# Kernel optimization log

Hardware: AMD Instinct MI355X
Metric: run time of the kernel (lower is better)

The kernel has to match this reference:

```python
import jax, jax.numpy as jnp
import numpy as np

B, T, NB = 8, 120, 40
VD, WD = 2053, 300
H, E, NH, HD = 512, 256, 8, 64
SEG, NSEG = 12, 10
IDX = np.round(np.linspace(SEG - 1, T - 1, NSEG)).astype(int)  # segment endpoints


def setup_inputs():
    keys = iter(jax.random.split(jax.random.key(0), 64))
    def w(*shape):
        return jax.random.normal(next(keys), shape, jnp.float32) * 0.02
    z = lambda *s: jnp.zeros(s, jnp.float32)
    return dict(
        videos=jax.random.normal(next(keys), (B, T, NB, VD), jnp.float32),
        sub_glove=jax.random.normal(next(keys), (B, WD), jnp.float32),
        obj_glove=jax.random.normal(next(keys), (B, WD), jnp.float32),
        W_ev=w(VD - 5, E), b_ev=z(E),
        W_el=w(5, E), b_el=z(E),
        W_ew=w(WD, E), b_ew=z(E),
        W_sp1=w(2 * E, E), b_sp1=z(E), w_sp2=w(E),
        W_s2o=w(NB, E), b_s2o=z(E),
        W_o2s=w(NB, E), b_o2s=z(E),
        W_tv=w(H, H), b_tv=z(H),
        Wq=w(H, H), bq=z(H), Wk=w(H, H), bk=z(H), Wv=w(H, H), bv=z(H), Wo=w(H, H), bo=z(H),
        g1=jnp.ones(H, jnp.float32), be1=z(H),
        Wf1=w(H, H), bf1=z(H), Wf2=w(H, H), bf2=z(H),
        g2=jnp.ones(H, jnp.float32), be2=z(H),
        W_tr=w(H, H), b_tr=z(H),
        W_tb1=w(2 * H, H), b_tb1=z(H), w_tb2=w(H),
        W_ih=w(4 * H, H), W_hh=w(4 * H, H), b_ih=z(4 * H), b_hh=z(4 * H),
        W_l1=w(2 * H, H), b_l1=z(H), w_l2=w(H),
    )


def reference(videos, sub_glove, obj_glove, W_ev, b_ev, W_el, b_el, W_ew, b_ew,
              W_sp1, b_sp1, w_sp2, W_s2o, b_s2o, W_o2s, b_o2s, W_tv, b_tv,
              Wq, bq, Wk, bk, Wv, bv, Wo, bo, g1, be1, Wf1, bf1, Wf2, bf2, g2, be2,
              W_tr, b_tr, W_tb1, b_tb1, w_tb2, W_ih, W_hh, b_ih, b_hh, W_l1, b_l1, w_l2):
    relu = jax.nn.relu
    # spatialAtt (vectorized over batch; dropout = identity, eval mode)
    ve = relu(videos[..., :VD - 5] @ W_ev + b_ev) + relu(videos[..., VD - 5:] @ W_el + b_el)  # [B,T,NB,E]
    sub_e = relu(sub_glove @ W_ew + b_ew)  # [B,E]
    obj_e = relu(obj_glove @ W_ew + b_ew)

    def attend(word):  # additive attention over bboxes per frame
        wb = jnp.broadcast_to(word[:, None, None, :], ve.shape)
        s = jnp.tanh(jnp.concatenate([ve, wb], -1) @ W_sp1 + b_sp1) @ w_sp2  # [B,T,NB]
        a = jax.nn.softmax(s, -1)
        return jnp.einsum('btn,btne->bte', a, ve), a

    sub_feat, sub_att = attend(sub_e)
    obj_feat, obj_att = attend(obj_e)
    s2o = relu(sub_att @ W_s2o + b_s2o)  # msg_sub2obj on attention weights [B,T,NB]->[B,T,E]
    o2s = relu(obj_att @ W_o2s + b_o2s)
    ori_x = jnp.concatenate([sub_feat + o2s, obj_feat + s2o], -1)  # [B,T,H]
    rel = jnp.concatenate([sub_e, obj_e], -1)[:, None, :]  # [B,1,H]

    def ln(zz, g, b):
        m = zz.mean(-1, keepdims=True)
        v = jnp.mean((zz - m) ** 2, -1, keepdims=True)
        return (zz - m) * jax.lax.rsqrt(v + 1e-5) * g + b

    # transform_visual + 1-layer post-norm TransformerEncoder (relu FFN, dropout=identity)
    x = relu(ori_x @ W_tv + b_tv)
    q = (x @ Wq + bq).reshape(B, T, NH, HD)
    k = (x @ Wk + bk).reshape(B, T, NH, HD)
    v = (x @ Wv + bv).reshape(B, T, NH, HD)
    att = jax.nn.softmax(jnp.einsum('bqhd,bkhd->bhqk', q, k) / np.float32(np.sqrt(HD)), -1)
    ao = jnp.einsum('bhqk,bkhd->bqhd', att, v).reshape(B, T, H) @ Wo + bo
    x = ln(x + ao, g1, be1)
    x = ln(x + relu(x @ Wf1 + bf1) @ Wf2 + bf2, g2, be2)
    within = x  # [B,T,H]

    seg_in = within[:, IDX, :]  # [B,NSEG,H]
    tr = relu(rel @ W_tr + b_tr)
    ctx = jnp.broadcast_to(tr, seg_in.shape)
    beta2 = jax.nn.softmax(jnp.tanh(jnp.concatenate([seg_in, ctx], -1) @ W_tb1 + b_tb1) @ w_tb2, -1)  # [B,NSEG]

    # torch-convention LSTM (gates i,f,g,o); note attention weights are NOT applied to input (vfeat=input)
    def step(carry, xt):
        h, c = carry
        gates = xt @ W_ih.T + h @ W_hh.T + b_ih + b_hh
        i, f, g_, o = jnp.split(gates, 4, -1)
        c = jax.nn.sigmoid(f) * c + jax.nn.sigmoid(i) * jnp.tanh(g_)
        h = jax.nn.sigmoid(o) * jnp.tanh(c)
        return (h, c), h

    (hT, cT), _ = jax.lax.scan(step, (jnp.zeros((B, H), within.dtype), jnp.zeros((B, H), within.dtype)),
                               seg_in.transpose(1, 0, 2))

    ctx2 = jnp.broadcast_to(hT[:, None, :], within.shape)
    beta1 = jax.nn.softmax(jnp.tanh(jnp.concatenate([within, ctx2], -1) @ W_l1 + b_l1) @ w_l2, -1)  # [B,T]
    temp = beta1 + jnp.repeat(beta2, SEG, axis=1)  # temp[:,i] = beta1[:,i] + beta2[:,i//12]
    output = jnp.einsum('bt,bth->bh', temp, within)  # [B,H]
    return output, hT, cT, sub_att, obj_att, beta1, beta2
```

## Files before the change

### kernel.cpp

```cpp
#include <hip/hip_runtime.h>
#include <cstddef>
#include <cstdint>

#define B_ 8
#define T_ 120
#define NB_ 40
#define VD_ 2053
#define E_ 256
#define H_ 512
#define M_ 38400
#define R_ 960

static constexpr size_t OFF_VE    = 0;
static constexpr size_t OFF_SSUB  = OFF_VE + (size_t)M_ * E_;
static constexpr size_t OFF_SOBJ  = OFF_SSUB + M_;
static constexpr size_t OFF_WBS   = OFF_SOBJ + M_;
static constexpr size_t OFF_WBO   = OFF_WBS + B_ * E_;
static constexpr size_t OFF_TBIAS = OFF_WBO + B_ * E_;
static constexpr size_t OFF_ORIX  = OFF_TBIAS + B_ * H_;
static constexpr size_t OFF_X     = OFF_ORIX + (size_t)R_ * H_;
static constexpr size_t OFF_Q     = OFF_X    + (size_t)R_ * H_;
static constexpr size_t OFF_K     = OFF_Q    + (size_t)R_ * H_;
static constexpr size_t OFF_V     = OFF_K    + (size_t)R_ * H_;
static constexpr size_t OFF_AO    = OFF_V    + (size_t)R_ * H_;
static constexpr size_t OFF_ATTN  = OFF_AO   + (size_t)R_ * H_;
static constexpr size_t OFF_X1    = OFF_ATTN + (size_t)R_ * H_;
static constexpr size_t OFF_F1    = OFF_X1   + (size_t)R_ * H_;
static constexpr size_t OFF_F2    = OFF_F1   + (size_t)R_ * H_;
static constexpr size_t OFF_WIN   = OFF_F2   + (size_t)R_ * H_;
static constexpr size_t OFF_WT    = OFF_WIN  + (size_t)R_ * H_;
static constexpr size_t OFF_Z2    = OFF_WT + (size_t)1024 * 2048;
static constexpr size_t OFF_H0    = OFF_Z2 + 128;
static constexpr size_t OFF_HB    = OFF_H0 + 3 * 4096;
static constexpr size_t OFF_L1    = OFF_HB + B_ * H_;
static constexpr size_t OFF_END0  = OFF_L1 + 960;
static constexpr size_t OFF_WIH   = (OFF_END0 + 3) & ~(size_t)3;
static constexpr size_t OFF_WHH   = OFF_WIH + 524288;
static constexpr size_t OFF_WL1B  = OFF_WHH + 524288;
static constexpr size_t OFF_WINBF = OFF_WL1B + 131072;
static constexpr size_t OFF_VEBF  = OFF_WINBF + 245760;
static constexpr size_t OFF_END   = OFF_VEBF + (size_t)M_ * E_ / 2;

static constexpr size_t O_OUT  = 0;
static constexpr size_t O_HT   = 4096;
static constexpr size_t O_CT   = 8192;
static constexpr size_t O_SATT = 12288;
static constexpr size_t O_OATT = 50688;
static constexpr size_t O_B1   = 89088;
static constexpr size_t O_B2   = 90048;

#define DEVFN __device__ __forceinline__

typedef __attribute__((ext_vector_type(8))) short short8;
typedef __attribute__((ext_vector_type(4))) float f32x4;

DEVFN float sigf(float x) { return 1.0f / (1.0f + __expf(-x)); }

DEVFN float fast_tanh(float x) {
  float e = __expf(2.f * x);
  return 1.f - 2.f / (e + 1.f);
}

DEVFN unsigned short f2bf(float x) {
  unsigned int u = __float_as_uint(x);
  u += 0x7FFFu + ((u >> 16) & 1u);
  return (unsigned short)(u >> 16);
}
DEVFN float bf2f(unsigned short u) { return __uint_as_float((unsigned int)u << 16); }

DEVFN short8 mk8(const float* f) {
  short8 r;
#pragma unroll
  for (int j = 0; j < 8; ++j) r[j] = (short)f2bf(f[j]);
  return r;
}

DEVFN float wredsum(float v) {
#pragma unroll
  for (int m = 32; m; m >>= 1) v += __shfl_xor(v, m);
  return v;
}
DEVFN float wredmax(float v) {
#pragma unroll
  for (int m = 32; m; m >>= 1) v = fmaxf(v, __shfl_xor(v, m));
  return v;
}

__global__ __launch_bounds__(256) void k_zero(float* p, int n) {
  int i = blockIdx.x * 256 + threadIdx.x;
  if (i < n) p[i] = 0.f;
}

__global__ __launch_bounds__(256) void k_small0(
    const float* __restrict__ sub_g, const float* __restrict__ obj_g,
    const float* __restrict__ W_ew, const float* __restrict__ b_ew,
    const float* __restrict__ W_sp1, const float* __restrict__ b_sp1,
    const float* __restrict__ W_tr, const float* __restrict__ b_tr,
    const float* __restrict__ W_tb1, const float* __restrict__ b_tb1,
    float* __restrict__ wbs, float* __restrict__ wbo, float* __restrict__ tbias) {
  int b = blockIdx.x, tid = threadIdx.x;
  __shared__ float sg[300], og[300], se[256], oe[256], trl[512];
  for (int i = tid; i < 300; i += 256) { sg[i] = sub_g[b * 300 + i]; og[i] = obj_g[b * 300 + i]; }
  __syncthreads();
  {
    float a1 = b_ew[tid], a2 = a1;
    for (int w = 0; w < 300; ++w) {
      float we = W_ew[w * 256 + tid];
      a1 += sg[w] * we; a2 += og[w] * we;
    }
    se[tid] = fmaxf(a1, 0.f); oe[tid] = fmaxf(a2, 0.f);
  }
  __syncthreads();
  {
    float a1 = b_sp1[tid], a2 = a1;
    for (int e = 0; e < 256; ++e) {
      float ww = W_sp1[(256 + e) * 256 + tid];
      a1 += se[e] * ww; a2 += oe[e] * ww;
    }
    wbs[b * 256 + tid] = a1; wbo[b * 256 + tid] = a2;
  }
  for (int jj = 0; jj < 2; ++jj) {
    int j = tid + jj * 256;
    float a = b_tr[j];
    for (int i = 0; i < 256; ++i) a += se[i] * W_tr[i * 512 + j];
    for (int i = 0; i < 256; ++i) a += oe[i] * W_tr[(256 + i) * 512 + j];
    trl[j] = fmaxf(a, 0.f);
  }
  __syncthreads();
  for (int jj = 0; jj < 2; ++jj) {
    int j = tid + jj * 256;
    float a = b_tb1[j];
    for (int i = 0; i < 512; ++i) a += trl[i] * W_tb1[(size_t)(512 + i) * 512 + j];
    tbias[b * 512 + j] = a;
  }
}

__global__ __launch_bounds__(256) void k_wprep(
    const float* __restrict__ W_ev, const float* __restrict__ W_tv,
    const float* __restrict__ Wq, const float* __restrict__ Wk,
    const float* __restrict__ Wv, const float* __restrict__ Wo,
    const float* __restrict__ Wf1, const float* __restrict__ Wf2,
    const float* __restrict__ W_sp1, const float* __restrict__ W_l1,
    const float* __restrict__ W_ih, const float* __restrict__ W_hh,
    unsigned short* __restrict__ wevbf, unsigned short* __restrict__ w7bf,
    unsigned short* __restrict__ wsp1bf, unsigned short* __restrict__ wl1bf,
    unsigned short* __restrict__ wihbf, unsigned short* __restrict__ whhbf,
    float* __restrict__ hz) {
  int bid = blockIdx.x, tid = threadIdx.x;
  __shared__ float t[64][65];
  if (bid < 128) {
    int kb = bid >> 2, nb = bid & 3;
#pragma unroll
    for (int i = 0; i < 16; ++i) {
      int idx = tid + 256 * i; int r = idx >> 6, c = idx & 63;
      t[r][c] = W_ev[(size_t)(kb * 64 + r) * 256 + nb * 64 + c];
    }
    __syncthreads();
#pragma unroll
    for (int i = 0; i < 16; ++i) {
      int idx = tid + 256 * i; int n = idx >> 6, kk = idx & 63;
      wevbf[(size_t)(nb * 64 + n) * 2048 + kb * 64 + kk] = f2bf(t[kk][n]);
    }
  } else if (bid < 576) {
    int b2 = bid - 128;
    int wsel = b2 >> 6, sub = b2 & 63;
    int kb = sub >> 3, nb = sub & 7;
    const float* src = wsel == 0 ? W_tv : wsel == 1 ? Wq : wsel == 2 ? Wk
                     : wsel == 3 ? Wv : wsel == 4 ? Wo : wsel == 5 ? Wf1 : Wf2;
    unsigned short* dst = w7bf + (size_t)wsel * 262144;
#pragma unroll
    for (int i = 0; i < 16; ++i) {
      int idx = tid + 256 * i; int r = idx >> 6, c = idx & 63;
      t[r][c] = src[(size_t)(kb * 64 + r) * 512 + nb * 64 + c];
    }
    __syncthreads();
#pragma unroll
    for (int i = 0; i < 16; ++i) {
      int idx = tid + 256 * i; int n = idx >> 6, kk = idx & 63;
      dst[(size_t)(nb * 64 + n) * 512 + kb * 64 + kk] = f2bf(t[kk][n]);
    }
  } else if (bid < 592) {
    int b2 = bid - 576;
    int kb = b2 >> 2, nb = b2 & 3;
#pragma unroll
    for (int i = 0; i < 16; ++i) {
      int idx = tid + 256 * i; int r = idx >> 6, c = idx & 63;
      t[r][c] = W_sp1[(size_t)(kb * 64 + r) * 256 + nb * 64 + c];
    }
    __syncthreads();
#pragma unroll
    for (int i = 0; i < 16; ++i) {
      int idx = tid + 256 * i; int n = idx >> 6, kk = idx & 63;
      wsp1bf[(size_t)(nb * 64 + n) * 256 + kb * 64 + kk] = f2bf(t[kk][n]);
    }
  } else if (bid < 656) {
    int b2 = bid - 592;
    int kb = b2 >> 3, nb = b2 & 7;
#pragma unroll
    for (int i = 0; i < 16; ++i) {
      int idx = tid + 256 * i; int r = idx >> 6, c = idx & 63;
      t[r][c] = W_l1[(size_t)(kb * 64 + r) * 512 + nb * 64 + c];
    }
    __syncthreads();
#pragma unroll
    for (int i = 0; i < 16; ++i) {
      int idx = tid + 256 * i; int n = idx >> 6, kk = idx & 63;
      wl1bf[(size_t)(nb * 64 + n) * 512 + kb * 64 + kk] = f2bf(t[kk][n]);
    }
  } else if (bid < 1680) {
    int i = (bid - 656) * 256 + tid;
    const float* s; unsigned short* d; int off;
    if (i < 131072) { s = W_ih; d = wihbf; off = i * 8; }
    else            { s = W_hh; d = whhbf; off = (i - 131072) * 8; }
    float f[8];
#pragma unroll
    for (int j = 0; j < 8; ++j) f[j] = s[off + j];
    *(short8*)(d + off) = mk8(f);
  } else {
    for (int i = tid; i < 12288; i += 256) hz[i] = 0.f;
  }
}

__global__ __launch_bounds__(256) void k_wconvT(const float* __restrict__ src,
                                                unsigned short* __restrict__ dst,
                                                int K, int N) {
  __shared__ float t[64][65];
  int nblk = N >> 6;
  int kb = blockIdx.x / nblk, nb = blockIdx.x - kb * nblk;
  int tid = threadIdx.x;
#pragma unroll
  for (int i = 0; i < 16; ++i) {
    int idx = tid + 256 * i;
    int r = idx >> 6, c = idx & 63;
    t[r][c] = src[(size_t)(kb * 64 + r) * N + nb * 64 + c];
  }
  __syncthreads();
#pragma unroll
  for (int i = 0; i < 16; ++i) {
    int idx = tid + 256 * i;
    int n = idx >> 6, kk = idx & 63;
    dst[(size_t)(nb * 64 + n) * K + kb * 64 + kk] = f2bf(t[kk][n]);
  }
}

__global__ __launch_bounds__(256) void k_wconv7(
    const float* __restrict__ w0, const float* __restrict__ w1,
    const float* __restrict__ w2, const float* __restrict__ w3,
    const float* __restrict__ w4, const float* __restrict__ w5,
    const float* __restrict__ w6, unsigned short* __restrict__ dstb) {
  __shared__ float t[64][65];
  int wsel = blockIdx.x >> 6, sub = blockIdx.x & 63;
  int kb = sub >> 3, nb = sub & 7;
  const float* src = wsel == 0 ? w0 : wsel == 1 ? w1 : wsel == 2 ? w2
                   : wsel == 3 ? w3 : wsel == 4 ? w4 : wsel == 5 ? w5 : w6;
  unsigned short* dst = dstb + (size_t)wsel * 262144;
  int tid = threadIdx.x;
#pragma unroll
  for (int i = 0; i < 16; ++i) {
    int idx = tid + 256 * i;
    int r = idx >> 6, c = idx & 63;
    t[r][c] = src[(size_t)(kb * 64 + r) * 512 + nb * 64 + c];
  }
  __syncthreads();
#pragma unroll
  for (int i = 0; i < 16; ++i) {
    int idx = tid + 256 * i;
    int n = idx >> 6, kk = idx & 63;
    dst[(size_t)(nb * 64 + n) * 512 + kb * 64 + kk] = f2bf(t[kk][n]);
  }
}

__global__ __launch_bounds__(256) void k_cvt2(const float* __restrict__ a,
                                              const float* __restrict__ b,
                                              unsigned short* __restrict__ da,
                                              unsigned short* __restrict__ db) {
  int i = blockIdx.x * 256 + threadIdx.x;
  const float* s; unsigned short* d; int off;
  if (i < 131072) { s = a; d = da; off = i * 8; }
  else            { s = b; d = db; off = (i - 131072) * 8; }
  float f[8];
#pragma unroll
  for (int j = 0; j < 8; ++j) f[j] = s[off + j];
  *(short8*)(d + off) = mk8(f);
}

__global__ __launch_bounds__(512) void k_gemm_ve_m97(
    const float* __restrict__ videos, const unsigned short* __restrict__ wtbf,
    const float* __restrict__ bev, const float* __restrict__ Wel,
    const float* __restrict__ bel, unsigned short* __restrict__ vebf) {
  __shared__ __align__(16) unsigned short lds[20480];
  int tid = threadIdx.x;
  int rowbase = blockIdx.x * 64;
  int lane = tid & 63, wid = tid >> 6;
  int l16 = lane & 15, lk = lane >> 4;

  int arow = tid >> 3, akc = tid & 7;
  const float* apA = videos + (size_t)(rowbase + arow) * VD_ + akc * 8;
  int dstA = arow * 64 + ((akc ^ (arow & 7)) * 8);
  const unsigned short* spB[4];
  int dstB[4];
#pragma unroll
  for (int i = 0; i < 4; ++i) {
    int g = tid + 512 * i;
    int n = g >> 3, kc = g & 7;
    spB[i] = wtbf + (size_t)n * 2048 + kc * 8;
    dstB[i] = 4096 + n * 64 + ((kc ^ (n & 7)) * 8);
  }
  float fa[8];
  short8 stB[4];
#pragma unroll
  for (int j = 0; j < 8; ++j) fa[j] = apA[j];
#pragma unroll
  for (int i = 0; i < 4; ++i) stB[i] = *(const short8*)(spB[i]);

  f32x4 acc[4][2] = {};
  for (int k0 = 0; k0 < 2048; k0 += 64) {
    short8 ha = mk8(fa);
    __syncthreads();
    *(short8*)(lds + dstA) = ha;
#pragma unroll
    for (int i = 0; i < 4; ++i) *(short8*)(lds + dstB[i]) = stB[i];
    __syncthreads();
    int kn = (k0 + 64 < 2048) ? k0 + 64 : 0;
#pragma unroll
    for (int j = 0; j < 8; ++j) fa[j] = apA[kn + j];
#pragma unroll
    for (int i = 0; i < 4; ++i) stB[i] = *(const short8*)(spB[i] + kn);
#pragma unroll
    for (int kk = 0; kk < 2; ++kk) {
      short8 a8[4], b8[2];
#pragma unroll
      for (int fm = 0; fm < 4; ++fm) {
        int row = fm * 16 + l16;
        a8[fm] = *(const short8*)(lds + row * 64 + (((kk * 4 + lk) ^ (row & 7)) * 8));
      }
#pragma unroll
      for (int fn = 0; fn < 2; ++fn) {
        int n = wid * 32 + fn * 16 + l16;
        b8[fn] = *(const short8*)(lds + 4096 + n * 64 + (((kk * 4 + lk) ^ (n & 7)) * 8));
      }
#pragma unroll
      for (int fm = 0; fm < 4; ++fm)
#pragma unroll
        for (int fn = 0; fn < 2; ++fn)
          acc[fm][fn] = __builtin_amdgcn_mfma_f32_16x16x32_bf16(
              a8[fm], b8[fn], acc[fm][fn], 0, 0, 0);
    }
  }
  float bevv[2], belv[2], w5[5][2];
#pragma unroll
  for (int fn = 0; fn < 2; ++fn) {
    int col = wid * 32 + fn * 16 + l16;
    bevv[fn] = bev[col]; belv[fn] = bel[col];
#pragma unroll
    for (int kk = 0; kk < 5; ++kk) w5[kk][fn] = Wel[kk * 256 + col];
  }
#pragma unroll
  for (int fm = 0; fm < 4; ++fm) {
#pragma unroll
    for (int r = 0; r < 4; ++r) {
      int grow = rowbase + fm * 16 + lk * 4 + r;
      const float* vt = videos + (size_t)grow * VD_ + 2048;
      float t0 = vt[0], t1 = vt[1], t2 = vt[2], t3 = vt[3], t4 = vt[4];
      unsigned short* vob = vebf + (size_t)grow * 256;
#pragma unroll
      for (int fn = 0; fn < 2; ++fn) {
        int col = wid * 32 + fn * 16 + l16;
        float s2 = belv[fn] + t0 * w5[0][fn] + t1 * w5[1][fn] + t2 * w5[2][fn] +
                   t3 * w5[3][fn] + t4 * w5[4][fn];
        float vvv = fmaxf(acc[fm][fn][r] + bevv[fn], 0.f) + fmaxf(s2, 0.f);
        vob[col] = f2bf(vvv);
      }
    }
  }
}

__global__ __launch_bounds__(256) void k_score_bf(
    const unsigned short* __restrict__ vebf, const unsigned short* __restrict__ wsp1,
    const float* __restrict__ w_sp2, const float* __restrict__ wbs,
    const float* __restrict__ wbo, float* __restrict__ s_sub,
    float* __restrict__ s_obj) {
  __shared__ float reds[4][64], redo_[4][64];
  int tid = threadIdx.x;
  int rowbase = blockIdx.x * 64;
  int lane = tid & 63, wid = tid >> 6;
  int l16 = lane & 15, lk = lane >> 4;
  const unsigned short* ap[4];
  const unsigned short* bp[4];
#pragma unroll
  for (int fm = 0; fm < 4; ++fm)
    ap[fm] = vebf + (size_t)(rowbase + fm * 16 + l16) * 256 + lk * 8;
#pragma unroll
  for (int fn = 0; fn < 4; ++fn)
    bp[fn] = wsp1 + (size_t)(wid * 64 + fn * 16 + l16) * 256 + lk * 8;
  f32x4 acc[4][4] = {};
#pragma unroll 2
  for (int k0 = 0; k0 < 256; k0 += 32) {
    short8 a8[4], b8[4];
#pragma unroll
    for (int fm = 0; fm < 4; ++fm) a8[fm] = *(const short8*)(ap[fm] + k0);
#pragma unroll
    for (int fn = 0; fn < 4; ++fn) b8[fn] = *(const short8*)(bp[fn] + k0);
#pragma unroll
    for (int fm = 0; fm < 4; ++fm)
#pragma unroll
      for (int fn = 0; fn < 4; ++fn)
        acc[fm][fn] = __builtin_amdgcn_mfma_f32_16x16x32_bf16(
            a8[fm], b8[fn], acc[fm][fn], 0, 0, 0);
  }
  int b = rowbase / 4800;
  float w2[4], bs[4], bo[4];
#pragma unroll
  for (int fn = 0; fn < 4; ++fn) {
    int col = wid * 64 + fn * 16 + l16;
    w2[fn] = w_sp2[col];
    bs[fn] = wbs[b * 256 + col];
    bo[fn] = wbo[b * 256 + col];
  }
  float ps[4][4], po[4][4];
#pragma unroll
  for (int fm = 0; fm < 4; ++fm)
#pragma unroll
    for (int r = 0; r < 4; ++r) {
      float aps = 0, apo = 0;
#pragma unroll
      for (int fn = 0; fn < 4; ++fn) {
        float t = acc[fm][fn][r];
        aps += fast_tanh(t + bs[fn]) * w2[fn];
        apo += fast_tanh(t + bo[fn]) * w2[fn];
      }
      ps[fm][r] = aps;
      po[fm][r] = apo;
    }
#pragma unroll
  for (int m = 1; m < 16; m <<= 1) {
#pragma unroll
    for (int fm = 0; fm < 4; ++fm)
#pragma unroll
      for (int r = 0; r < 4; ++r) {
        ps[fm][r] += __shfl_xor(ps[fm][r], m);
        po[fm][r] += __shfl_xor(po[fm][r], m);
      }
  }
  if (l16 == 0) {
#pragma unroll
    for (int fm = 0; fm < 4; ++fm)
#pragma unroll
      for (int r = 0; r < 4; ++r) {
        int row = fm * 16 + lk * 4 + r;
        reds[wid][row] = ps[fm][r];
        redo_[wid][row] = po[fm][r];
      }
  }
  __syncthreads();
  if (tid < 64) {
    float s1 = reds[0][tid] + reds[1][tid] + reds[2][tid] + reds[3][tid];
    float s2 = redo_[0][tid] + redo_[1][tid] + redo_[2][tid] + redo_[3][tid];
    s_sub[rowbase + tid] = s1;
    s_obj[rowbase + tid] = s2;
  }
}

__global__ __launch_bounds__(256) void k_attend_bf(
    const float* __restrict__ s_sub, const float* __restrict__ s_obj,
    const unsigned short* __restrict__ vebf, const float* __restrict__ W_s2o,
    const float* __restrict__ b_s2o, const float* __restrict__ W_o2s,
    const float* __restrict__ b_o2s, float* __restrict__ out_satt,
    float* __restrict__ out_oatt, float* __restrict__ orix) {
  int row = blockIdx.x;
  int tid = threadIdx.x;
  __shared__ float alds[2][40];
  int wv = tid >> 6, lane = tid & 63;
  if (wv < 2) {
    const float* sarr = (wv ? s_obj : s_sub) + row * 40;
    float v = (lane < 40) ? sarr[lane] : -1e30f;
    float mx = wredmax(v);
    float e = (lane < 40) ? __expf(v - mx) : 0.f;
    float sm = wredsum(e);
    float p = e / sm;
    if (lane < 40) {
      alds[wv][lane] = p;
      (wv ? out_oatt : out_satt)[row * 40 + lane] = p;
    }
  }
  __syncthreads();
  int e = tid;
  const unsigned short* vrow = vebf + (size_t)row * 40 * 256;
  float sf = 0, of = 0, s2o = b_s2o[e], o2s = b_o2s[e];
  for (int n = 0; n < 40; ++n) {
    float as = alds[0][n], aob = alds[1][n];
    float vv = bf2f(vrow[n * 256 + e]);
    sf += as * vv;
    of += aob * vv;
    s2o += as * W_s2o[n * 256 + e];
    o2s += aob * W_o2s[n * 256 + e];
  }
  s2o = fmaxf(s2o, 0.f);
  o2s = fmaxf(o2s, 0.f);
  orix[(size_t)row * 512 + e] = sf + o2s;
  orix[(size_t)row * 512 + 256 + e] = of + s2o;
}

__global__ __launch_bounds__(256) void k_gemm_ve_mfma(
    const float* __restrict__ videos, const unsigned short* __restrict__ wtbf,
    const float* __restrict__ bev, const float* __restrict__ Wel,
    const float* __restrict__ bel, float* __restrict__ ve) {
  int tid = threadIdx.x;
  int rowbase = blockIdx.x * 64;
  int lane = tid & 63, wid = tid >> 6;
  int l16 = lane & 15, lk = lane >> 4;
  const float* ap[4];
  const unsigned short* bp[4];
#pragma unroll
  for (int fm = 0; fm < 4; ++fm)
    ap[fm] = videos + (size_t)(rowbase + fm * 16 + l16) * VD_ + lk * 8;
#pragma unroll
  for (int fn = 0; fn < 4; ++fn)
    bp[fn] = wtbf + (size_t)(wid * 64 + fn * 16 + l16) * 2048 + lk * 8;
  f32x4 acc[4][4] = {};
  for (int k0 = 0; k0 < 2048; k0 += 64) {
// ... 120 lines not shown
    float p = e / sm;
    if (lane < 40) {
      alds[wv][lane] = p;
      (wv ? out_oatt : out_satt)[row * 40 + lane] = p;
    }
  }
  __syncthreads();
  int e = tid;
  const float* vrow = ve + (size_t)row * 40 * 256;
  float sf = 0, of = 0, s2o = b_s2o[e], o2s = b_o2s[e];
  for (int n = 0; n < 40; ++n) {
    float as = alds[0][n], aob = alds[1][n];
    float vv = vrow[n * 256 + e];
    sf += as * vv;
    of += aob * vv;
    s2o += as * W_s2o[n * 256 + e];
    o2s += aob * W_o2s[n * 256 + e];
  }
  s2o = fmaxf(s2o, 0.f);
  o2s = fmaxf(o2s, 0.f);
  orix[(size_t)row * 512 + e] = sf + o2s;
  orix[(size_t)row * 512 + 256 + e] = of + s2o;
}

__global__ __launch_bounds__(256) void k_gemm_h(
    const float* __restrict__ A, const unsigned short* __restrict__ WT,
    const float* __restrict__ b0, const float* __restrict__ b1,
    const float* __restrict__ b2, float* __restrict__ Cbase, int ntiles,
    int relu) {
  int tid = threadIdx.x;
  int bid = blockIdx.x;
  int mt = bid / ntiles, nt = bid - mt * ntiles;
  int rowbase = mt * 64;
  int lane = tid & 63, wid = tid >> 6;
  int wrow = wid >> 1, wcol = wid & 1;
  int l16 = lane & 15, lk = lane >> 4;
  const float* ap[2];
  const unsigned short* bp[2];
#pragma unroll
  for (int fm = 0; fm < 2; ++fm)
    ap[fm] = A + (size_t)(rowbase + wrow * 32 + fm * 16 + l16) * 512 + lk * 8;
#pragma unroll
  for (int fn = 0; fn < 2; ++fn)
    bp[fn] = WT + (size_t)(nt * 64 + wcol * 32 + fn * 16 + l16) * 512 + lk * 8;
  f32x4 acc[2][2] = {};
  for (int k0 = 0; k0 < 512; k0 += 64) {
#pragma unroll
    for (int kk = 0; kk < 2; ++kk) {
      int ko = k0 + kk * 32;
      short8 a8[2], b8[2];
#pragma unroll
      for (int fm = 0; fm < 2; ++fm) {
        float4 x = *(const float4*)(ap[fm] + ko);
        float4 y = *(const float4*)(ap[fm] + ko + 4);
        float f[8] = {x.x, x.y, x.z, x.w, y.x, y.y, y.z, y.w};
        a8[fm] = mk8(f);
      }
#pragma unroll
      for (int fn = 0; fn < 2; ++fn) b8[fn] = *(const short8*)(bp[fn] + ko);
#pragma unroll
      for (int fm = 0; fm < 2; ++fm)
#pragma unroll
        for (int fn = 0; fn < 2; ++fn)
          acc[fm][fn] = __builtin_amdgcn_mfma_f32_16x16x32_bf16(
              a8[fm], b8[fn], acc[fm][fn], 0, 0, 0);
    }
  }
#pragma unroll
  for (int fn = 0; fn < 2; ++fn) {
    int cg = nt * 64 + wcol * 32 + fn * 16 + l16;
    int third = cg >> 9, c = cg & 511;
    const float* bb = third == 0 ? b0 : (third == 1 ? b1 : b2);
    float bv = bb[c];
    float* outp = Cbase + (size_t)third * ((size_t)R_ * H_);
#pragma unroll
    for (int fm = 0; fm < 2; ++fm) {
#pragma unroll
      for (int r = 0; r < 4; ++r) {
        int grow = rowbase + wrow * 32 + fm * 16 + lk * 4 + r;
        float v = acc[fm][fn][r] + bv;
        if (relu) v = fmaxf(v, 0.f);
        outp[(size_t)grow * 512 + c] = v;
      }
    }
  }
}

__global__ __launch_bounds__(256) void k_xproj(
    const float* __restrict__ win, const unsigned short* __restrict__ wih,
    const float* __restrict__ b_ih, const float* __restrict__ b_hh,
    float* __restrict__ gx) {
  int bid = blockIdx.x;
  int mt = bid >> 5, nt = bid & 31;
  int tid = threadIdx.x;
  int lane = tid & 63, wid = tid >> 6;
  int wrow = wid >> 1, wcol = wid & 1;
  int l16 = lane & 15, lk = lane >> 4;
  const float* ap[2];
  bool av[2];
#pragma unroll
  for (int fm = 0; fm < 2; ++fm) {
    int base = mt * 64 + wrow * 32 + fm * 16;
    av[fm] = base < 80;
    int grow = base + l16;
    int s = grow >> 3, b = grow & 7;
    ap[fm] = av[fm] ? (win + (size_t)(b * 120 + 11 + 12 * s) * 512 + lk * 8)
                    : win;
  }
  const unsigned short* bp[2];
#pragma unroll
  for (int fn = 0; fn < 2; ++fn)
    bp[fn] = wih + (size_t)(nt * 64 + wcol * 32 + fn * 16 + l16) * 512 + lk * 8;
  f32x4 acc[2][2] = {};
  for (int k0 = 0; k0 < 512; k0 += 64) {
#pragma unroll
    for (int kk = 0; kk < 2; ++kk) {
      int ko = k0 + kk * 32;
      short8 a8[2], b8[2];
#pragma unroll
      for (int fm = 0; fm < 2; ++fm) {
        if (av[fm]) {
          float4 x = *(const float4*)(ap[fm] + ko);
          float4 y = *(const float4*)(ap[fm] + ko + 4);
          float f[8] = {x.x, x.y, x.z, x.w, y.x, y.y, y.z, y.w};
          a8[fm] = mk8(f);
        } else {
          a8[fm] = short8{0, 0, 0, 0, 0, 0, 0, 0};
        }
      }
#pragma unroll
      for (int fn = 0; fn < 2; ++fn) b8[fn] = *(const short8*)(bp[fn] + ko);
#pragma unroll
      for (int fm = 0; fm < 2; ++fm)
#pragma unroll
        for (int fn = 0; fn < 2; ++fn)
          acc[fm][fn] = __builtin_amdgcn_mfma_f32_16x16x32_bf16(
              a8[fm], b8[fn], acc[fm][fn], 0, 0, 0);
    }
  }
#pragma unroll
  for (int fn = 0; fn < 2; ++fn) {
    int cg = nt * 64 + wcol * 32 + fn * 16 + l16;
    float bv = b_ih[cg] + b_hh[cg];
#pragma unroll
    for (int fm = 0; fm < 2; ++fm) {
      if (!av[fm]) continue;
#pragma unroll
      for (int r = 0; r < 4; ++r) {
        int grow = mt * 64 + wrow * 32 + fm * 16 + lk * 4 + r;
        if (grow < 80) gx[(size_t)grow * 2048 + cg] = acc[fm][fn][r] + bv;
      }
    }
  }
}

__global__ __launch_bounds__(128) void k_lstm_step(
    const float* __restrict__ hin, const unsigned short* __restrict__ whh,
    const float* __restrict__ gx, int s, float* __restrict__ hout,
    float* __restrict__ c_st) {
  int jb = blockIdx.x;
  int tid = threadIdx.x;
  int lane = tid & 63, kw = tid >> 6;
  int l16 = lane & 15, lk = lane >> 4;
  const float* ap = hin + (size_t)l16 * 512 + kw * 256 + lk * 8;
  const unsigned short* bp[4];
#pragma unroll
  for (int fn = 0; fn < 4; ++fn)
    bp[fn] = whh + (size_t)(fn * 512 + jb * 16 + l16) * 512 + kw * 256 + lk * 8;
  f32x4 acc[4] = {};
  for (int k0 = 0; k0 < 256; k0 += 64) {
#pragma unroll
    for (int kk = 0; kk < 2; ++kk) {
      int ko = k0 + kk * 32;
      float4 x = *(const float4*)(ap + ko);
      float4 y = *(const float4*)(ap + ko + 4);
      float f[8] = {x.x, x.y, x.z, x.w, y.x, y.y, y.z, y.w};
      short8 a8 = mk8(f);
#pragma unroll
      for (int fn = 0; fn < 4; ++fn) {
        short8 b8 = *(const short8*)(bp[fn] + ko);
        acc[fn] = __builtin_amdgcn_mfma_f32_16x16x32_bf16(a8, b8, acc[fn], 0, 0, 0);
      }
    }
  }
  __shared__ float part[4][64][4];
  if (kw == 1) {
#pragma unroll
    for (int fn = 0; fn < 4; ++fn)
#pragma unroll
      for (int r = 0; r < 4; ++r) part[fn][lane][r] = acc[fn][r];
  }
  __syncthreads();
  if (kw == 0 && lk < 2) {
    int j = jb * 16 + l16;
#pragma unroll
    for (int r = 0; r < 4; ++r) {
      int b = lk * 4 + r;
      const float* g = gx + (size_t)(s * 8 + b) * 2048;
      float gi = acc[0][r] + part[0][lane][r] + g[j];
      float gf = acc[1][r] + part[1][lane][r] + g[512 + j];
      float gg = acc[2][r] + part[2][lane][r] + g[1024 + j];
      float go = acc[3][r] + part[3][lane][r] + g[1536 + j];
      float c = sigf(gf) * c_st[b * 512 + j] + sigf(gi) * fast_tanh(gg);
      c_st[b * 512 + j] = c;
      hout[b * 512 + j] = sigf(go) * fast_tanh(c);
    }
  }
}

__global__ __launch_bounds__(256) void k_mha(const float* __restrict__ qb,
                                             const float* __restrict__ kb,
                                             const float* __restrict__ vb,
                                             float* __restrict__ ao) {
  int bh = blockIdx.x & 63, qc = blockIdx.x >> 6;
  int b = bh >> 3, h = bh & 7;
  __shared__ float ks[120 * 65];
  __shared__ float vs[120 * 65];
  __shared__ float ps[4][128];
  int tid = threadIdx.x;
  for (int i = 0; i < 30; ++i) {
    int idx = tid + 256 * i;
    int t = idx >> 6, d = idx & 63;
    size_t g = (size_t)(b * 120 + t) * 512 + h * 64 + d;
    ks[t * 65 + d] = kb[g];
    vs[t * 65 + d] = vb[g];
  }
  __syncthreads();
  int wv = tid >> 6, lane = tid & 63;
  for (int i = qc * 30 + wv; i < qc * 30 + 30; i += 4) {
    const float* qrow = qb + (size_t)(b * 120 + i) * 512 + h * 64;
    float s1 = 0, s2 = 0;
    for (int d = 0; d < 64; ++d) {
      float qd = qrow[d];
      s1 += qd * ks[lane * 65 + d];
      if (lane < 56) s2 += qd * ks[(lane + 64) * 65 + d];
    }
    s1 *= 0.125f;
    s2 *= 0.125f;
    if (lane >= 56) s2 = -1e30f;
    float mx = wredmax(fmaxf(s1, s2));
    float e1 = __expf(s1 - mx);
    float e2 = (lane < 56) ? __expf(s2 - mx) : 0.f;
    float sm = wredsum(e1 + e2);
    ps[wv][lane] = e1;
    ps[wv][64 + lane] = e2;
    float o = 0;
    for (int j = 0; j < 120; ++j) o += ps[wv][j] * vs[j * 65 + lane];
    ao[(size_t)(b * 120 + i) * 512 + h * 64 + lane] = o / sm;
  }
}

__global__ __launch_bounds__(256) void k_ln(const float* __restrict__ a,
                                            const float* __restrict__ bsrc,
                                            const float* __restrict__ g,
                                            const float* __restrict__ be,
                                            float* __restrict__ out,
                                            unsigned short* __restrict__ bfout) {
  int row = blockIdx.x * 4 + (threadIdx.x >> 6);
  int lane = threadIdx.x & 63;
  const float* pa = a + (size_t)row * 512;
  const float* pb = bsrc + (size_t)row * 512;
  float z[8];
  float s = 0;
#pragma unroll
  for (int ii = 0; ii < 8; ++ii) {
    int e = lane + 64 * ii;
    z[ii] = pa[e] + pb[e];
    s += z[ii];
  }
  float mean = wredsum(s) * (1.f / 512.f);
  float v = 0;
#pragma unroll
  for (int ii = 0; ii < 8; ++ii) {
    float d = z[ii] - mean;
    v += d * d;
  }
  float rstd = rsqrtf(wredsum(v) * (1.f / 512.f) + 1e-5f);
#pragma unroll
  for (int ii = 0; ii < 8; ++ii) {
    int e = lane + 64 * ii;
    float val = (z[ii] - mean) * rstd * g[e] + be[e];
    out[(size_t)row * 512 + e] = val;
    if (bfout) bfout[(size_t)row * 512 + e] = f2bf(val);
  }
}

__global__ __launch_bounds__(256) void k_hbias(const float* __restrict__ hT,
                                               const float* __restrict__ W_l1,
                                               const float* __restrict__ b_l1,
                                               float* __restrict__ hb) {
  int b = blockIdx.x >> 1, half = blockIdx.x & 1;
  int tid = threadIdx.x;
  __shared__ float hl[512];
  for (int i = tid; i < 512; i += 256) hl[i] = hT[b * 512 + i];
  __syncthreads();
  int j = half * 256 + tid;
  float a = b_l1[j];
  for (int i = 0; i < 512; ++i) a += hl[i] * W_l1[(size_t)(512 + i) * 512 + j];
  hb[b * 512 + j] = a;
}

__global__ __launch_bounds__(256) void k_beta2(
    const float* __restrict__ within, const float* __restrict__ W_tb1,
    const float* __restrict__ w_tb2, const float* __restrict__ tbias,
    float* __restrict__ z2) {
  int bid = blockIdx.x;
// ... 98 lines not shown
  __syncthreads();
  float v[4] = {0, 0, 0, 0};
  for (int jj = 0; jj < 2; ++jj) {
    int j = tid + jj * 256;
    float hbv = hb[b * 512 + j];
    float a0 = hbv, a1 = hbv, a2 = hbv, a3 = hbv;
    for (int i = 0; i < 512; ++i) {
      float ww = W_l1[(size_t)i * 512 + j];
      a0 += xr[0][i] * ww;
      a1 += xr[1][i] * ww;
      a2 += xr[2][i] * ww;
      a3 += xr[3][i] * ww;
    }
    float wl = w_l2[j];
    v[0] += fast_tanh(a0) * wl;
    v[1] += fast_tanh(a1) * wl;
    v[2] += fast_tanh(a2) * wl;
    v[3] += fast_tanh(a3) * wl;
  }
#pragma unroll
  for (int r = 0; r < 4; ++r) red[r][tid] = v[r];
  __syncthreads();
  for (int s = 128; s; s >>= 1) {
    if (tid < s)
      for (int r = 0; r < 4; ++r) red[r][tid] += red[r][tid + s];
    __syncthreads();
  }
  if (tid < 4) l1[r0 + tid] = red[tid][0];
}

__global__ __launch_bounds__(256) void k_final(
    const float* __restrict__ l1, const float* __restrict__ z2,
    const float* __restrict__ within, const float* __restrict__ hT,
    const float* __restrict__ cT, float* __restrict__ dout) {
  int b = blockIdx.x;
  int tid = threadIdx.x;
  __shared__ float temp[120];
  __shared__ float b2[10];
  int wv = tid >> 6, lane = tid & 63;
  if (wv == 1) {
    float v = (lane < 10) ? z2[b * 10 + lane] : -1e30f;
    float mx = wredmax(v);
    float e = (lane < 10) ? __expf(v - mx) : 0.f;
    float sm = wredsum(e);
    if (lane < 10) {
      float p = e / sm;
      b2[lane] = p;
      dout[O_B2 + b * 10 + lane] = p;
    }
  }
  if (wv == 0) {
    float v1 = l1[b * 120 + lane];
    float v2 = (lane + 64 < 120) ? l1[b * 120 + 64 + lane] : -1e30f;
    float mx = wredmax(fmaxf(v1, v2));
    float e1 = __expf(v1 - mx);
    float e2 = (lane + 64 < 120) ? __expf(v2 - mx) : 0.f;
    float sm = wredsum(e1 + e2);
    float p1 = e1 / sm;
    dout[O_B1 + b * 120 + lane] = p1;
    temp[lane] = p1;
    if (lane + 64 < 120) {
      float p2 = e2 / sm;
      dout[O_B1 + b * 120 + 64 + lane] = p2;
      temp[64 + lane] = p2;
    }
  }
  __syncthreads();
  for (int t = tid; t < 120; t += 256) temp[t] += b2[t / 12];
  __syncthreads();
  for (int hh = tid; hh < 512; hh += 256) {
    float o = 0;
    for (int t = 0; t < 120; ++t) o += temp[t] * within[(size_t)(b * 120 + t) * 512 + hh];
    dout[O_OUT + b * 512 + hh] = o;
    dout[O_HT + b * 512 + hh] = hT[b * 512 + hh];
    dout[O_CT + b * 512 + hh] = cT[b * 512 + hh];
  }
}

extern "C" void kernel_launch(void* const* d_in, const int* in_sizes, int n_in,
                              void* d_out, int out_size, void* d_ws, size_t ws_size,
                              hipStream_t stream) {
  const float* videos = (const float*)d_in[0];
  const float* sub_g  = (const float*)d_in[1];
  const float* obj_g  = (const float*)d_in[2];
  const float* W_ev   = (const float*)d_in[3];
  const float* b_ev   = (const float*)d_in[4];
  const float* W_el   = (const float*)d_in[5];
  const float* b_el   = (const float*)d_in[6];
  const float* W_ew   = (const float*)d_in[7];
  const float* b_ew   = (const float*)d_in[8];
  const float* W_sp1  = (const float*)d_in[9];
  const float* b_sp1  = (const float*)d_in[10];
  const float* w_sp2  = (const float*)d_in[11];
  const float* W_s2o  = (const float*)d_in[12];
  const float* b_s2o  = (const float*)d_in[13];
  const float* W_o2s  = (const float*)d_in[14];
  const float* b_o2s  = (const float*)d_in[15];
  const float* W_tv   = (const float*)d_in[16];
  const float* b_tv   = (const float*)d_in[17];
  const float* Wq     = (const float*)d_in[18];
  const float* bq     = (const float*)d_in[19];
  const float* Wk     = (const float*)d_in[20];
  const float* bk     = (const float*)d_in[21];
  const float* Wv     = (const float*)d_in[22];
  const float* bv     = (const float*)d_in[23];
  const float* Wo     = (const float*)d_in[24];
  const float* bo     = (const float*)d_in[25];
  const float* g1     = (const float*)d_in[26];
  const float* be1    = (const float*)d_in[27];
  const float* Wf1    = (const float*)d_in[28];
  const float* bf1    = (const float*)d_in[29];
  const float* Wf2    = (const float*)d_in[30];
  const float* bf2    = (const float*)d_in[31];
  const float* g2     = (const float*)d_in[32];
  const float* be2    = (const float*)d_in[33];
  const float* W_tr   = (const float*)d_in[34];
  const float* b_tr   = (const float*)d_in[35];
  const float* W_tb1  = (const float*)d_in[36];
  const float* b_tb1  = (const float*)d_in[37];
  const float* w_tb2  = (const float*)d_in[38];
  const float* W_ih   = (const float*)d_in[39];
  const float* W_hh   = (const float*)d_in[40];
  const float* b_ih   = (const float*)d_in[41];
  const float* b_hh   = (const float*)d_in[42];
  const float* W_l1   = (const float*)d_in[43];
  const float* b_l1   = (const float*)d_in[44];
  const float* w_l2   = (const float*)d_in[45];

  float* out = (float*)d_out;
  float* w = (float*)d_ws;

  float* ve_p   = w + OFF_VE;
  float* ssub_p = w + OFF_SSUB;
  float* sobj_p = w + OFF_SOBJ;
  float* wbs_p  = w + OFF_WBS;
  float* wbo_p  = w + OFF_WBO;
  float* tb_p   = w + OFF_TBIAS;
  float* orix_p = w + OFF_ORIX;
  float* x_p    = w + OFF_X;
  float* q_p    = w + OFF_Q;
  float* k_p    = w + OFF_K;
  float* v_p    = w + OFF_V;
  float* ao_p   = w + OFF_AO;
  float* attn_p = w + OFF_ATTN;
  float* x1_p   = w + OFF_X1;
  float* f1_p   = w + OFF_F1;
  float* f2_p   = w + OFF_F2;
  float* win_p  = w + OFF_WIN;
  float* z2_p   = w + OFF_Z2;
  float* h_p    = w + OFF_H0;
  float* c_p    = h_p + 2 * 4096;
  float* hb_p   = w + OFF_HB;
  float* l1_p   = w + OFF_L1;

  unsigned short* wtbase = (unsigned short*)(w + OFF_WT);
  unsigned short* wevbf = wtbase;
  unsigned short* w7bf  = wtbase + 524288;
  unsigned short* wtvbf = w7bf;
  unsigned short* wqbf  = w7bf + 1 * 262144;
  unsigned short* wobf  = w7bf + 4 * 262144;
  unsigned short* wf1bf = w7bf + 5 * 262144;
  unsigned short* wf2bf = w7bf + 6 * 262144;
  unsigned short* wsp1bf = w7bf + 7 * 262144;
  unsigned short* wihbf  = (unsigned short*)(w + OFF_WIH);
  unsigned short* whhbf  = (unsigned short*)(w + OFF_WHH);
  unsigned short* wl1bf  = (unsigned short*)(w + OFF_WL1B);
  unsigned short* winbf_p = (unsigned short*)(w + OFF_WINBF);
  unsigned short* vebf_p = (unsigned short*)(w + OFF_VEBF);
  float* gx_p = w + OFF_Q;
  const bool big = ws_size >= (size_t)OFF_END * 4;

  if (big) {
    k_wprep<<<1681, 256, 0, stream>>>(W_ev, W_tv, Wq, Wk, Wv, Wo, Wf1, Wf2,
                                      W_sp1, W_l1, W_ih, W_hh, wevbf, w7bf,
                                      wsp1bf, wl1bf, wihbf, whhbf, h_p);
    k_small0<<<8, 256, 0, stream>>>(sub_g, obj_g, W_ew, b_ew, W_sp1, b_sp1,
                                    W_tr, b_tr, W_tb1, b_tb1, wbs_p, wbo_p, tb_p);
    k_gemm_ve_m97<<<600, 512, 0, stream>>>(videos, wevbf, b_ev, W_el, b_el,
                                           vebf_p);
    k_score_bf<<<600, 256, 0, stream>>>(vebf_p, wsp1bf, w_sp2, wbs_p, wbo_p,
                                        ssub_p, sobj_p);
    k_attend_bf<<<960, 256, 0, stream>>>(ssub_p, sobj_p, vebf_p, W_s2o, b_s2o,
                                         W_o2s, b_o2s, out + O_SATT,
                                         out + O_OATT, orix_p);
    k_gemm_h<<<120, 256, 0, stream>>>(orix_p, wtvbf, b_tv, b_tv, b_tv, x_p, 8, 1);
    k_gemm_h<<<360, 256, 0, stream>>>(x_p, wqbf, bq, bk, bv, q_p, 24, 0);
    k_mha<<<256, 256, 0, stream>>>(q_p, k_p, v_p, ao_p);
    k_gemm_h<<<120, 256, 0, stream>>>(ao_p, wobf, bo, bo, bo, attn_p, 8, 0);
    k_ln<<<240, 256, 0, stream>>>(x_p, attn_p, g1, be1, x1_p, nullptr);
    k_gemm_h<<<120, 256, 0, stream>>>(x1_p, wf1bf, bf1, bf1, bf1, f1_p, 8, 1);
    k_gemm_h<<<120, 256, 0, stream>>>(f1_p, wf2bf, bf2, bf2, bf2, f2_p, 8, 0);
    k_ln<<<240, 256, 0, stream>>>(x1_p, f2_p, g2, be2, win_p, winbf_p);
    k_xproj<<<64, 256, 0, stream>>>(win_p, wihbf, b_ih, b_hh, gx_p);
    k_beta2<<<80, 256, 0, stream>>>(win_p, W_tb1, w_tb2, tb_p, z2_p);
    for (int s = 0; s < 10; ++s) {
      float* hin = h_p + (s & 1) * 4096;
      float* hout = h_p + ((s & 1) ^ 1) * 4096;
      k_lstm_step<<<32, 128, 0, stream>>>(hin, whhbf, gx_p, s, hout, c_p);
    }
    k_hbias<<<16, 256, 0, stream>>>(h_p, W_l1, b_l1, hb_p);
    k_beta1_bf<<<15, 256, 0, stream>>>(winbf_p, wl1bf, w_l2, hb_p, l1_p);
    k_final<<<8, 256, 0, stream>>>(l1_p, z2_p, win_p, h_p, c_p, out);
  } else {
    unsigned short* wihbf_a = (unsigned short*)(w + OFF_Q + 163840);
    unsigned short* whhbf_a = (unsigned short*)(w + OFF_Q + 688128);
    k_zero<<<48, 256, 0, stream>>>(h_p, 3 * 4096);
    k_small0<<<8, 256, 0, stream>>>(sub_g, obj_g, W_ew, b_ew, W_sp1, b_sp1,
                                    W_tr, b_tr, W_tb1, b_tb1, wbs_p, wbo_p, tb_p);
    k_wconvT<<<128, 256, 0, stream>>>(W_ev, wevbf, 2048, 256);
    k_wconv7<<<448, 256, 0, stream>>>(W_tv, Wq, Wk, Wv, Wo, Wf1, Wf2, w7bf);
    k_gemm_ve_mfma<<<600, 256, 0, stream>>>(videos, wevbf, b_ev, W_el, b_el, ve_p);
    k_score<<<1200, 256, 0, stream>>>(ve_p, W_sp1, w_sp2, wbs_p, wbo_p, ssub_p, sobj_p);
    k_attend<<<960, 256, 0, stream>>>(ssub_p, sobj_p, ve_p, W_s2o, b_s2o, W_o2s,
                                      b_o2s, out + O_SATT, out + O_OATT, orix_p);
    k_gemm_h<<<120, 256, 0, stream>>>(orix_p, wtvbf, b_tv, b_tv, b_tv, x_p, 8, 1);
    k_gemm_h<<<360, 256, 0, stream>>>(x_p, wqbf, bq, bk, bv, q_p, 24, 0);
    k_mha<<<256, 256, 0, stream>>>(q_p, k_p, v_p, ao_p);
    k_gemm_h<<<120, 256, 0, stream>>>(ao_p, wobf, bo, bo, bo, attn_p, 8, 0);
    k_ln<<<240, 256, 0, stream>>>(x_p, attn_p, g1, be1, x1_p, nullptr);
    k_gemm_h<<<120, 256, 0, stream>>>(x1_p, wf1bf, bf1, bf1, bf1, f1_p, 8, 1);
    k_gemm_h<<<120, 256, 0, stream>>>(f1_p, wf2bf, bf2, bf2, bf2, f2_p, 8, 0);
    k_ln<<<240, 256, 0, stream>>>(x1_p, f2_p, g2, be2, win_p, nullptr);
    k_cvt2<<<1024, 256, 0, stream>>>(W_ih, W_hh, wihbf_a, whhbf_a);
    k_xproj<<<64, 256, 0, stream>>>(win_p, wihbf_a, b_ih, b_hh, gx_p);
    k_beta2<<<80, 256, 0, stream>>>(win_p, W_tb1, w_tb2, tb_p, z2_p);
    for (int s = 0; s < 10; ++s) {
      float* hin = h_p + (s & 1) * 4096;
      float* hout = h_p + ((s & 1) ^ 1) * 4096;
      k_lstm_step<<<32, 128, 0, stream>>>(hin, whhbf_a, gx_p, s, hout, c_p);
    }
    k_hbias<<<16, 256, 0, stream>>>(h_p, W_l1, b_l1, hb_p);
    k_beta1<<<240, 256, 0, stream>>>(win_p, W_l1, w_l2, hb_p, l1_p);
    k_final<<<8, 256, 0, stream>>>(l1_p, z2_p, win_p, h_p, c_p, out);
  }
}
```

Measured before the change: 661.0 us.

## Fuse LSTM steps with grid barrier and split ve GEMM across column halves

The ten per-step LSTM launches plus the h-bias kernel are replaced by one persistent 32-block kernel that synchronises steps through an atomic grid barrier in workspace, reset in the weight-prep kernel. The hidden-bias computation is folded into the tail of that kernel. Separately, the ve GEMM drops from 512-thread blocks covering all 256 columns to 256-thread blocks covering 128 columns, doubling the grid to 1200 blocks with smaller LDS. This aims to cut launch overhead on the serial LSTM chain and improve occupancy for the big GEMM. The costs are spin-wait barrier cost, which relies on all 32 blocks being co-resident, and the A tile of videos being read twice.

```diff
diff --git a/kernel.cpp b/kernel.cpp
--- a/kernel.cpp
+++ b/kernel.cpp
@@ -33,7 +33,8 @@
 static constexpr size_t OFF_H0    = OFF_Z2 + 128;
 static constexpr size_t OFF_HB    = OFF_H0 + 3 * 4096;
 static constexpr size_t OFF_L1    = OFF_HB + B_ * H_;
-static constexpr size_t OFF_END0  = OFF_L1 + 960;
+static constexpr size_t OFF_BAR   = OFF_L1 + 960;
+static constexpr size_t OFF_END0  = OFF_BAR + 4;
 static constexpr size_t OFF_WIH   = (OFF_END0 + 3) & ~(size_t)3;
 static constexpr size_t OFF_WHH   = OFF_WIH + 524288;
 static constexpr size_t OFF_WL1B  = OFF_WHH + 524288;
@@ -145,7 +146,7 @@
     unsigned short* __restrict__ wevbf, unsigned short* __restrict__ w7bf,
     unsigned short* __restrict__ wsp1bf, unsigned short* __restrict__ wl1bf,
     unsigned short* __restrict__ wihbf, unsigned short* __restrict__ whhbf,
-    float* __restrict__ hz) {
+    float* __restrict__ hz, unsigned int* __restrict__ bar) {
   int bid = blockIdx.x, tid = threadIdx.x;
   __shared__ float t[64][65];
   if (bid < 128) {
@@ -218,6 +219,7 @@
     *(short8*)(d + off) = mk8(f);
   } else {
     for (int i = tid; i < 12288; i += 256) hz[i] = 0.f;
+    if (tid == 0) *bar = 0u;
   }
 }
 
@@ -284,46 +286,61 @@
   *(short8*)(d + off) = mk8(f);
 }
 
-__global__ __launch_bounds__(512) void k_gemm_ve_m97(
+__global__ __launch_bounds__(256) void k_gemm_ve_m97(
     const float* __restrict__ videos, const unsigned short* __restrict__ wtbf,
     const float* __restrict__ bev, const float* __restrict__ Wel,
     const float* __restrict__ bel, unsigned short* __restrict__ vebf) {
-  __shared__ __align__(16) unsigned short lds[20480];
-  int tid = threadIdx.x;
-  int rowbase = blockIdx.x * 64;
+  __shared__ __align__(16) unsigned short lds[12288];
+  int tid = threadIdx.x;
+  int bid = blockIdx.x;
+  int chunk = bid >> 4, within = bid & 15;
+  int cb = within >> 3, r8 = within & 7;
+  int rowbase = (chunk * 8 + r8) * 64;
+  int colbase = cb * 128;
   int lane = tid & 63, wid = tid >> 6;
   int l16 = lane & 15, lk = lane >> 4;
 
-  int arow = tid >> 3, akc = tid & 7;
-  const float* apA = videos + (size_t)(rowbase + arow) * VD_ + akc * 8;
-  int dstA = arow * 64 + ((akc ^ (arow & 7)) * 8);
+  const float* spA[2];
+  int dstA[2];
+#pragma unroll
+  for (int i = 0; i < 2; ++i) {
+    int g = tid + 256 * i;
+    int row = g >> 3, kc = g & 7;
+    spA[i] = videos + (size_t)(rowbase + row) * VD_ + kc * 8;
+    dstA[i] = row * 64 + ((kc ^ (row & 7)) * 8);
+  }
   const unsigned short* spB[4];
   int dstB[4];
 #pragma unroll
   for (int i = 0; i < 4; ++i) {
-    int g = tid + 512 * i;
+    int g = tid + 256 * i;
     int n = g >> 3, kc = g & 7;
-    spB[i] = wtbf + (size_t)n * 2048 + kc * 8;
+    spB[i] = wtbf + (size_t)(colbase + n) * 2048 + kc * 8;
     dstB[i] = 4096 + n * 64 + ((kc ^ (n & 7)) * 8);
   }
-  float fa[8];
+  float fa[2][8];
   short8 stB[4];
 #pragma unroll
-  for (int j = 0; j < 8; ++j) fa[j] = apA[j];
+  for (int i = 0; i < 2; ++i)
+#pragma unroll
+    for (int j = 0; j < 8; ++j) fa[i][j] = spA[i][j];
 #pragma unroll
   for (int i = 0; i < 4; ++i) stB[i] = *(const short8*)(spB[i]);
 
   f32x4 acc[4][2] = {};
   for (int k0 = 0; k0 < 2048; k0 += 64) {
-    short8 ha = mk8(fa);
+    short8 ha0 = mk8(fa[0]), ha1 = mk8(fa[1]);
     __syncthreads();
-    *(short8*)(lds + dstA) = ha;
+    *(short8*)(lds + dstA[0]) = ha0;
+    *(short8*)(lds + dstA[1]) = ha1;
 #pragma unroll
     for (int i = 0; i < 4; ++i) *(short8*)(lds + dstB[i]) = stB[i];
     __syncthreads();
     int kn = (k0 + 64 < 2048) ? k0 + 64 : 0;
 #pragma unroll
-    for (int j = 0; j < 8; ++j) fa[j] = apA[kn + j];
+    for (int i = 0; i < 2; ++i)
+#pragma unroll
+      for (int j = 0; j < 8; ++j) fa[i][j] = spA[i][kn + j];
 #pragma unroll
     for (int i = 0; i < 4; ++i) stB[i] = *(const short8*)(spB[i] + kn);
 #pragma unroll
@@ -350,7 +367,7 @@
   float bevv[2], belv[2], w5[5][2];
 #pragma unroll
   for (int fn = 0; fn < 2; ++fn) {
-    int col = wid * 32 + fn * 16 + l16;
+    int col = colbase + wid * 32 + fn * 16 + l16;
     bevv[fn] = bev[col]; belv[fn] = bel[col];
 #pragma unroll
     for (int kk = 0; kk < 5; ++kk) w5[kk][fn] = Wel[kk * 256 + col];
@@ -365,7 +382,7 @@
       unsigned short* vob = vebf + (size_t)grow * 256;
 #pragma unroll
       for (int fn = 0; fn < 2; ++fn) {
-        int col = wid * 32 + fn * 16 + l16;
+        int col = colbase + wid * 32 + fn * 16 + l16;
         float s2 = belv[fn] + t0 * w5[0][fn] + t1 * w5[1][fn] + t2 * w5[2][fn] +
                    t3 * w5[3][fn] + t4 * w5[4][fn];
         float vvv = fmaxf(acc[fm][fn][r] + bevv[fn], 0.f) + fmaxf(s2, 0.f);
@@ -792,6 +809,79 @@
       }
     }
   }
+}
+
+__global__ __launch_bounds__(128) void k_lstm_all(
+    const unsigned short* __restrict__ whh, const float* __restrict__ gx,
+    float* __restrict__ h0, float* __restrict__ h1, float* __restrict__ c_st,
+    const float* __restrict__ W_l1, const float* __restrict__ b_l1,
+    float* __restrict__ hb, unsigned int* __restrict__ bar) {
+  int jb = blockIdx.x;
+  int tid = threadIdx.x;
+  int lane = tid & 63, kw = tid >> 6;
+  int l16 = lane & 15, lk = lane >> 4;
+  const unsigned short* bp[4];
+#pragma unroll
+  for (int fn = 0; fn < 4; ++fn)
+    bp[fn] = whh + (size_t)(fn * 512 + jb * 16 + l16) * 512 + kw * 256 + lk * 8;
+  __shared__ float part[4][64][4];
+  for (int s = 0; s < 10; ++s) {
+    const float* hin = (s & 1) ? h1 : h0;
+    float* hout = (s & 1) ? h0 : h1;
+    const float* ap = hin + (size_t)l16 * 512 + kw * 256 + lk * 8;
+    f32x4 acc[4] = {};
+    for (int k0 = 0; k0 < 256; k0 += 64) {
+#pragma unroll
+      for (int kk = 0; kk < 2; ++kk) {
+        int ko = k0 + kk * 32;
+        float4 x = *(const float4*)(ap + ko);
+        float4 y = *(const float4*)(ap + ko + 4);
+        float f[8] = {x.x, x.y, x.z, x.w, y.x, y.y, y.z, y.w};
+        short8 a8 = mk8(f);
+#pragma unroll
+        for (int fn = 0; fn < 4; ++fn) {
+          short8 b8 = *(const short8*)(bp[fn] + ko);
+          acc[fn] = __builtin_amdgcn_mfma_f32_16x16x32_bf16(a8, b8, acc[fn], 0, 0, 0);
+        }
+      }
+    }
+    if (kw == 1) {
+#pragma unroll
+      for (int fn = 0; fn < 4; ++fn)
+#pragma unroll
+        for (int r = 0; r < 4; ++r) part[fn][lane][r] = acc[fn][r];
+    }
+    __syncthreads();
+    if (kw == 0 && lk < 2) {
+      int j = jb * 16 + l16;
+#pragma unroll
+      for (int r = 0; r < 4; ++r) {
+        int b = lk * 4 + r;
+        const float* g = gx + (size_t)(s * 8 + b) * 2048;
+        float gi = acc[0][r] + part[0][lane][r] + g[j];
+        float gf = acc[1][r] + part[1][lane][r] + g[512 + j];
+        float gg = acc[2][r] + part[2][lane][r] + g[1024 + j];
+        float go = acc[3][r] + part[3][lane][r] + g[1536 + j];
+        float c = sigf(gf) * c_st[b * 512 + j] + sigf(gi) * fast_tanh(gg);
+        c_st[b * 512 + j] = c;
+        hout[b * 512 + j] = sigf(go) * fast_tanh(c);
+      }
+    }
+    __syncthreads();
+    __threadfence();
+    __syncthreads();
+    if (tid == 0) {
+      atomicAdd(bar, 1u);
+      while (atomicAdd(bar, 0u) < 32u * (unsigned)(s + 1)) {}
+    }
+    __syncthreads();
+    __threadfence();
+  }
+  int b = tid >> 4, j = jb * 16 + (tid & 15);
+  float a = b_l1[j];
+  const float* hr = h0 + b * 512;
+  for (int i = 0; i < 512; ++i) a += hr[i] * W_l1[(size_t)(512 + i) * 512 + j];
+  hb[b * 512 + j] = a;
 }
 
 __global__ __launch_bounds__(128) void k_lstm_step(
@@ -1196,6 +1286,7 @@
   float* c_p    = h_p + 2 * 4096;
   float* hb_p   = w + OFF_HB;
   float* l1_p   = w + OFF_L1;
+  unsigned int* bar_p = (unsigned int*)(w + OFF_BAR);
 
   unsigned short* wtbase = (unsigned short*)(w + OFF_WT);
   unsigned short* wevbf = wtbase;
@@ -1217,11 +1308,11 @@
   if (big) {
     k_wprep<<<1681, 256, 0, stream>>>(W_ev, W_tv, Wq, Wk, Wv, Wo, Wf1, Wf2,
                                       W_sp1, W_l1, W_ih, W_hh, wevbf, w7bf,
-                                      wsp1bf, wl1bf, wihbf, whhbf, h_p);
+                                      wsp1bf, wl1bf, wihbf, whhbf, h_p, bar_p);
     k_small0<<<8, 256, 0, stream>>>(sub_g, obj_g, W_ew, b_ew, W_sp1, b_sp1,
                                     W_tr, b_tr, W_tb1, b_tb1, wbs_p, wbo_p, tb_p);
-    k_gemm_ve_m97<<<600, 512, 0, stream>>>(videos, wevbf, b_ev, W_el, b_el,
-                                           vebf_p);
+    k_gemm_ve_m97<<<1200, 256, 0, stream>>>(videos, wevbf, b_ev, W_el, b_el,
+                                            vebf_p);
     k_score_bf<<<600, 256, 0, stream>>>(vebf_p, wsp1bf, w_sp2, wbs_p, wbo_p,
                                         ssub_p, sobj_p);
     k_attend_bf<<<960, 256, 0, stream>>>(ssub_p, sobj_p, vebf_p, W_s2o, b_s2o,
@@ -1237,12 +1328,8 @@
     k_ln<<<240, 256, 0, stream>>>(x1_p, f2_p, g2, be2, win_p, winbf_p);
     k_xproj<<<64, 256, 0, stream>>>(win_p, wihbf, b_ih, b_hh, gx_p);
     k_beta2<<<80, 256, 0, stream>>>(win_p, W_tb1, w_tb2, tb_p, z2_p);
-    for (int s = 0; s < 10; ++s) {
-      float* hin = h_p + (s & 1) * 4096;
-      float* hout = h_p + ((s & 1) ^ 1) * 4096;
-      k_lstm_step<<<32, 128, 0, stream>>>(hin, whhbf, gx_p, s, hout, c_p);
-    }
-    k_hbias<<<16, 256, 0, stream>>>(h_p, W_l1, b_l1, hb_p);
+    k_lstm_all<<<32, 128, 0, stream>>>(whhbf, gx_p, h_p, h_p + 4096, c_p,
+                                       W_l1, b_l1, hb_p, bar_p);
     k_beta1_bf<<<15, 256, 0, stream>>>(winbf_p, wl1bf, w_l2, hb_p, l1_p);
     k_final<<<8, 256, 0, stream>>>(l1_p, z2_p, win_p, h_p, c_p, out);
   } else {
```

Result: slower. 708.9 us (+7.2%).
